# Optimization experiments

Hardware: AMD Instinct MI355X
Metric: run time of the kernel (lower is better)

The kernel has to match this reference:

```python
import jax, jax.numpy as jnp
import numpy as np
from jax import lax

B, IC, OC, H, W_DIM, K = 8, 64, 64, 256, 512, 3
BLUR_1D = [1.0, 3.0, 3.0, 1.0]
FACTOR = 2
GAIN = 1.0


def _blur_kernel():
    # setup_resample_kernel: outer product of 1D kernel, normalized to sum 1
    k = np.asarray(BLUR_1D, dtype=np.float32)
    k = np.outer(k, k)
    k = k / np.sum(k)
    return k  # [4,4]


def setup_inputs() -> dict:
    key = jax.random.key(0)
    ks = jax.random.split(key, 5)
    x = jax.random.normal(ks[0], (B, IC, H, H), dtype=jnp.float32)
    w = jax.random.normal(ks[1], (B, W_DIM), dtype=jnp.float32)
    # init_std = 1.0 for both weights since lrmul = 1.0
    w_conv = jax.random.normal(ks[2], (K, K, IC, OC), dtype=jnp.float32)
    w_dense = jax.random.normal(ks[3], (W_DIM, IC), dtype=jnp.float32)
    b_mod = jnp.zeros((IC,), dtype=jnp.float32)
    return {"x": x, "w": w, "w_conv": w_conv, "w_dense": w_dense, "b_mod": b_mod}


def reference(x, w, w_conv, w_dense, b_mod):
    k = w_conv.shape[0]
    ic, oc = w_conv.shape[2], w_conv.shape[3]

    # runtime coefs (equalized lr): he_std = gain / sqrt(fan_in), lrmul = 1
    coef_conv = 1.0 / np.sqrt(k * k * ic)
    coef_dense = 1.0 / np.sqrt(w.shape[1])

    # style = Dense(w) + bias (linear act, gain 1) + 1.0   -> [B, IC]
    style = w @ (coef_dense * w_dense) + b_mod + 1.0

    # modulate: [B,k,k,IC,OC]
    wmod = (coef_conv * w_conv)[None] * style[:, None, None, :, None]
    # demodulate over (kh, kw, ic)
    d = lax.rsqrt(jnp.sum(jnp.square(wmod), axis=(1, 2, 3)) + 1e-8)  # [B,OC]
    wmod = wmod * d[:, None, None, None, :]

    # per-sample grouped transposed conv (upsample x2) == lhs-dilated cross-corr
    # with the unflipped modulated weight, padding k-1 on each side.
    w_oihw = jnp.transpose(wmod, (0, 4, 3, 1, 2))  # [B,OC,IC,k,k]

    def up_conv(xb, wb):
        return lax.conv_general_dilated(
            xb[None], wb, window_strides=(1, 1),
            padding=[(k - 1, k - 1), (k - 1, k - 1)],
            lhs_dilation=(FACTOR, FACTOR),
            dimension_numbers=("NCHW", "OIHW", "NCHW"))[0]

    y = jax.vmap(up_conv)(x, w_oihw)  # [B,OC,(H-1)*2+k,(W-1)*2+k] = [B,OC,513,513]

    # upfirdn blur: kernel scaled by gain * factor**2, pad0 = pad1 = 1,
    # true convolution (kernel flipped in reference) applied depthwise.
    kb = jnp.asarray(_blur_kernel() * (GAIN * FACTOR ** 2))  # [4,4]
    fw = kb[::-1, ::-1][None, None]  # [1,1,4,4]
    b_, c_, s1, s2 = y.shape
    y = lax.conv_general_dilated(
        y.reshape(b_ * c_, 1, s1, s2), fw, window_strides=(1, 1),
        padding=[(1, 1), (1, 1)],
        dimension_numbers=("NCHW", "OIHW", "NCHW"))
    # output spatial: s1 + 2 - 4 + 1 = 2H
    return y.reshape(b_, c_, y.shape[2], y.shape[3])
```

## Files before the change

### kernel.cpp

```cpp
#include <hip/hip_runtime.h>

#define NB 8
#define IC 64
#define OC 64
#define HH 256
#define WD 512
#define PP 258

typedef __bf16 bf16x8 __attribute__((ext_vector_type(8)));
typedef float f32x16 __attribute__((ext_vector_type(16)));
typedef float f32x2 __attribute__((ext_vector_type(2)));

__device__ inline void compute_E(const float* __restrict__ w_conv, float stv,
                                 int oc, float E[6][6]) {
  const float coef_conv = 1.0f / 24.0f;
  const float s = stv * coef_conv;
  const int ic = threadIdx.x & 63;

  float wm[3][3];
  float ssq = 0.f;
  #pragma unroll
  for (int kh = 0; kh < 3; ++kh)
    #pragma unroll
    for (int kw = 0; kw < 3; ++kw) {
      float v = w_conv[((kh * 3 + kw) * IC + ic) * OC + oc] * s;
      wm[kh][kw] = v;
      ssq += v * v;
    }
  #pragma unroll
  for (int off = 32; off > 0; off >>= 1) ssq += __shfl_xor(ssq, off);
  const float d = rsqrtf(ssq + 1e-8f);
  #pragma unroll
  for (int kh = 0; kh < 3; ++kh)
    #pragma unroll
    for (int kw = 0; kw < 3; ++kw) wm[kh][kw] *= d;

  const float g[4] = {0.25f, 0.75f, 0.75f, 0.25f};
  #pragma unroll
  for (int a = 0; a < 6; ++a)
    #pragma unroll
    for (int c = 0; c < 6; ++c) {
      float acc = 0.f;
      #pragma unroll
      for (int dh = 0; dh < 3; ++dh) {
        int u = a - dh;
        if (u < 0 || u > 3) continue;
        #pragma unroll
        for (int dw = 0; dw < 3; ++dw) {
          int v = c - dw;
          if (v < 0 || v > 3) continue;
          acc = fmaf(wm[dh][dw], g[u] * g[v], acc);
        }
      }
      E[a][c] = acc;
    }
}

__device__ inline float style_of(const float* __restrict__ w,
                                 const float* __restrict__ w_dense,
                                 const float* __restrict__ b_mod, int b,
                                 int ic) {
  const float coef_dense = 0.044194173824159216f;
  const float* wr = w + b * WD;
  float acc = 0.f;
  for (int k = 0; k < WD; ++k) acc = fmaf(wr[k], w_dense[k * IC + ic], acc);
  return acc * coef_dense + b_mod[ic] + 1.0f;
}

__global__ __launch_bounds__(64) void pwfs_kernel(
    const float* __restrict__ w, const float* __restrict__ w_dense,
    const float* __restrict__ b_mod, const float* __restrict__ w_conv,
    __bf16* __restrict__ PWf) {
  const int oc = blockIdx.x;
  const int b = blockIdx.y;
  const int ic = threadIdx.x;

  float stv = style_of(w, w_dense, b_mod, b, ic);
  float E[6][6];
  compute_E(w_conv, stv, oc, E);

  const int ks = ic >> 4;
  const int h = (ic >> 3) & 1;
  const int e = ic & 7;
  const int lane = (oc & 31) + 32 * h;
  const int ocg = oc >> 5;

  #pragma unroll
  for (int pp = 0; pp < 2; ++pp)
    #pragma unroll
    for (int pq = 0; pq < 2; ++pq) {
      const int ph = pp * 2 + pq;
      #pragma unroll
      for (int j = 0; j < 3; ++j)
        #pragma unroll
        for (int l = 0; l < 3; ++l) {
          const int tap = j * 3 + l;
          float val = E[2 * j + 1 - pp][2 * l + 1 - pq];
          size_t off =
              ((size_t)(((((b * 4 + ph) * 9 + tap) * 2 + ocg) * 4 + ks)) * 64 +
               lane) * 8 + e;
          PWf[off] = (__bf16)val;
        }
    }
}

#define XS 268
__global__ __launch_bounds__(256) void xtp_kernel(const float* __restrict__ x,
                                                  __bf16* __restrict__ xTg) {
  __shared__ unsigned short buf[64 * XS];
  const int tid = threadIdx.x;
  const int m = blockIdx.x;
  const int b = blockIdx.y;

  if (m == 256) {
    uint4 z = make_uint4(0, 0, 0, 0);
    for (int i = tid; i < 8224; i += 256) {
      int pix = i >> 3;
      int sub = i & 7;
      int pr, pc;
      if (pix < 258) {
        pr = 0; pc = pix;
      } else if (pix < 516) {
        pr = 257; pc = pix - 258;
      } else {
        int rem = pix - 516;
        pr = 1 + (rem >> 1);
        pc = (rem & 1) ? 257 : 0;
      }
      *(uint4*)(xTg + ((size_t)(b * PP + pr) * PP + pc) * 64 + sub * 8) = z;
    }
    return;
  }

  const int ln = tid & 63, grp = tid >> 6;
  #pragma unroll
  for (int p = 0; p < 16; ++p) {
    const int ic = p * 4 + grp;
    float4 v = *(const float4*)(x + ((size_t)(b * 64 + ic) * 256 + m) * 256 +
                                ln * 4);
    ushort4 u4;
    u4.x = __builtin_bit_cast(unsigned short, (__bf16)v.x);
    u4.y = __builtin_bit_cast(unsigned short, (__bf16)v.y);
    u4.z = __builtin_bit_cast(unsigned short, (__bf16)v.z);
    u4.w = __builtin_bit_cast(unsigned short, (__bf16)v.w);
    *(ushort4*)&buf[ic * XS + ln * 4] = u4;
  }
  __syncthreads();
  #pragma unroll
  for (int it = 0; it < 8; ++it) {
    int pix = it * 32 + (tid >> 3);
    int g = tid & 7;
    bf16x8 o;
    #pragma unroll
    for (int e = 0; e < 8; ++e)
      o[e] = __builtin_bit_cast(__bf16, buf[(g * 8 + e) * XS + pix]);
    *(bf16x8*)(xTg + ((size_t)(b * PP + m + 1) * PP + (pix + 1)) * 64 +
               g * 8) = o;
  }
}

#define CMT 16
#define CNT 32
#define XR 18
#define XC 34

__device__ __forceinline__ void loadA(const bf16x8* __restrict__ Av, int phb,
                                      int ocg, int ks, int l, int lane,
                                      bf16x8 A[3][2]) {
  #pragma unroll
  for (int j = 0; j < 3; ++j) {
    const int tap = j * 3 + l;
    #pragma unroll
    for (int pq = 0; pq < 2; ++pq)
      A[j][pq] =
          Av[(size_t)((((phb + pq) * 9 + tap) * 2 + ocg) * 4 + ks) * 64 + lane];
  }
}

#define GLD_LDS(src, dst)                                                \
  __builtin_amdgcn_global_load_lds(                                      \
      (const __attribute__((address_space(1))) void*)(src),              \
      (__attribute__((address_space(3))) void*)(dst), 16, 0, 0)

__device__ __forceinline__ void stage_tile(const __bf16* __restrict__ xTg,
                                           int b, int m0, int n0,
                                           __bf16* xsbuf, int wv, int lane) {
  const int r0 = (18 * wv) >> 4;
  const int r1 = (18 * (wv + 1)) >> 4;
  for (int row = r0; row < r1; ++row) {
    const size_t srow = (size_t)(b * PP + m0 + row) * PP;
    __bf16* ldsrow = xsbuf + row * (XC * 64);
    #pragma unroll
    for (int q = 0; q < 4; ++q) {
      int pix = q * 8 + (lane >> 3);
      int g = (lane & 7) ^ (pix & 7);
      const __bf16* src = xTg + (srow + (n0 + pix)) * 64 + g * 8;
      GLD_LDS(src, ldsrow + q * 512);
    }
    if (lane < 16) {
      int pix = 32 + (lane >> 3);
      int g = (lane & 7) ^ (pix & 7);
      const __bf16* src = xTg + (srow + (n0 + pix)) * 64 + g * 8;
      GLD_LDS(src, ldsrow + 2048);
    }
  }
}

__global__ __launch_bounds__(1024) void conv32p_kernel(
    const __bf16* __restrict__ xTg, const __bf16* __restrict__ PWf,
    float* __restrict__ out) {
  __shared__ __bf16 xs[2][XR * XC * 64];

  const int tid = threadIdx.x;
  const int lane = tid & 63;
  const int wv = tid >> 6;
  const int pp = wv & 1;
  const int rh = wv >> 1;

  const int bid = blockIdx.x;
  const int ngrp = bid & 1;
  const int mtile = (bid >> 1) & 15;
  const int ocg = (bid >> 5) & 1;
  const int b = bid >> 6;
  const int m0 = mtile * CMT;

  const int ln31 = lane & 31;
  const int lh = lane >> 5;
  const bf16x8* Av = (const bf16x8*)PWf;
  const int phb = b * 4 + pp * 2;

  stage_tile(xTg, b, m0, ngrp * 128, &xs[0][0], wv, lane);
  asm volatile("s_waitcnt vmcnt(0)" ::: "memory");
  __builtin_amdgcn_s_barrier();

  #pragma unroll 1
  for (int t = 0; t < 4; ++t) {
    const int n0 = ngrp * 128 + t * 32;
    if (t < 3)
      stage_tile(xTg, b, m0, n0 + 32, &xs[(t + 1) & 1][0], wv, lane);

    const __bf16* xb = &xs[t & 1][0];

    f32x16 acc[2][2];
    #pragma unroll
    for (int mw = 0; mw < 2; ++mw)
      #pragma unroll
      for (int pq = 0; pq < 2; ++pq)
        #pragma unroll
        for (int e = 0; e < 16; ++e) acc[mw][pq][e] = 0.f;

    int ks = 0, l = 0;
    #pragma unroll 1
    for (int it = 0; it < 12; ++it) {
      bf16x8 Ac[3][2];
      loadA(Av, phb, ocg, ks, l, lane, Ac);

      bf16x8 Bf[4];
      const int col_t = ln31 + l;
      const int gneed = ks * 2 + lh;
      #pragma unroll
      for (int r = 0; r < 4; ++r) {
        const int lds_row = 2 * rh + r;
        Bf[r] = *(const bf16x8*)(xb + ((lds_row * XC + col_t) * 8 +
                                       (gneed ^ (col_t & 7))) * 8);
      }

      __builtin_amdgcn_s_setprio(1);
      #pragma unroll
      for (int r = 0; r < 4; ++r) {
        #pragma unroll
        for (int j = 0; j < 3; ++j) {
          const int mw = r - j;
          if (mw == 0 || mw == 1) {
            acc[mw][0] = __builtin_amdgcn_mfma_f32_32x32x16_bf16(
                Ac[j][0], Bf[r], acc[mw][0], 0, 0, 0);
            acc[mw][1] = __builtin_amdgcn_mfma_f32_32x32x16_bf16(
                Ac[j][1], Bf[r], acc[mw][1], 0, 0, 0);
          }
        }
      }
      __builtin_amdgcn_s_setprio(0);

      l = (l == 2) ? 0 : l + 1;
      ks = (l == 0) ? (ks + 1) & 3 : ks;
    }

    #pragma unroll
    for (int mw = 0; mw < 2; ++mw) {
      const int p = 2 * (m0 + 2 * rh + mw) + pp;
      #pragma unroll
      for (int rr = 0; rr < 16; ++rr) {
        const int oc_loc = (rr & 3) + 8 * (rr >> 2) + 4 * lh;
        const int oc = ocg * 32 + oc_loc;
        size_t off =
            ((size_t)(b * 64 + oc) * 512 + p) * 512 + 2 * n0 + 2 * ln31;
        f32x2 v2;
        v2[0] = acc[mw][0][rr];
        v2[1] = acc[mw][1][rr];
        __builtin_nontemporal_store(v2, (f32x2*)(out + off));
      }
    }

    asm volatile("s_waitcnt vmcnt(63)" ::: "memory");
    __builtin_amdgcn_s_barrier();
  }
}

__global__ __launch_bounds__(64) void pw_kernel(
    const float* __restrict__ w, const float* __restrict__ w_dense,
    const float* __restrict__ b_mod, const float* __restrict__ w_conv,
    float* __restrict__ PW) {
  const int oc = blockIdx.x;
  const int b = blockIdx.y;
  const int ic = threadIdx.x;
  float stv = style_of(w, w_dense, b_mod, b, ic);
  float E[6][6];
  compute_E(w_conv, stv, oc, E);
  #pragma unroll
  for (int pp = 0; pp < 2; ++pp)
    #pragma unroll
    for (int pq = 0; pq < 2; ++pq)
      #pragma unroll
      for (int j = 0; j < 3; ++j)
        #pragma unroll
        for (int l = 0; l < 3; ++l)
          PW[(((size_t)((b * 4 + pp * 2 + pq) * OC + oc) * IC + ic) * 9) +
             j * 3 + l] = E[2 * j + 1 - pp][2 * l + 1 - pq];
}

#define MT 16
#define NT 64
#define ICC 8
#define XROWS 18
#define XCOLS 66
#define XSTRIDE 68

__global__ __launch_bounds__(256) void conv_kernel(
    const float* __restrict__ x, const float* __restrict__ PW,
    float* __restrict__ out) {
  __shared__ float lds_x[ICC][XROWS][XSTRIDE];
  __shared__ float lds_w[4][ICC][9][4];

  const int tid = threadIdx.x;
  const int tn = tid & 15;
  const int tm = tid >> 4;
  const int bx = blockIdx.x;
  const int ntile = bx & 3;
  const int mtile = bx >> 2;
  const int ocg = blockIdx.y;
  const int b = blockIdx.z;
  const int m0 = mtile * MT;
  const int n0 = ntile * NT;

  float acc[4][4][4];
  #pragma unroll
  for (int o = 0; o < 4; ++o)
    #pragma unroll
    for (int ph = 0; ph < 4; ++ph)
      #pragma unroll
      for (int s = 0; s < 4; ++s) acc[o][ph][s] = 0.f;

  for (int ic0 = 0; ic0 < IC; ic0 += ICC) {
    __syncthreads();
    for (int ici = 0; ici < ICC; ++ici) {
      const float* xsrc = x + (size_t)(b * IC + ic0 + ici) * HH * HH;
      for (int rc = tid; rc < XROWS * XCOLS; rc += 256) {
        int r = rc / XCOLS;
        int c = rc - r * XCOLS;
        int gr = m0 - 1 + r;
        int gc = n0 - 1 + c;
        float v = 0.f;
        if ((unsigned)gr < HH && (unsigned)gc < HH) v = xsrc[gr * HH + gc];
        lds_x[ici][r][c] = v;
      }
    }
    for (int idx = tid; idx < 4 * ICC * 9 * 4; idx += 256) {
      int o = idx / (ICC * 9 * 4);
      int rem = idx - o * (ICC * 9 * 4);
      int ici = rem / 36;
      int r2 = rem - ici * 36;
      int t = r2 >> 2;
      int ph = r2 & 3;
      lds_w[o][ici][t][ph] =
          PW[(((size_t)((b * 4 + ph) * OC + (ocg * 4 + o)) * IC +
               (ic0 + ici)) * 9) + t];
    }
    __syncthreads();
    for (int ici = 0; ici < ICC; ++ici) {
      #pragma unroll
      for (int j = 0; j < 3; ++j) {
        const float* xr = &lds_x[ici][tm + j][tn * 4];
        float4 a4 = *(const float4*)xr;
        float2 a2 = *(const float2*)(xr + 4);
        float xv[6] = {a4.x, a4.y, a4.z, a4.w, a2.x, a2.y};
        #pragma unroll
        for (int l = 0; l < 3; ++l) {
          #pragma unroll
          for (int o = 0; o < 4; ++o) {
            float4 wv = *(const float4*)&lds_w[o][ici][j * 3 + l][0];
            #pragma unroll
            for (int s = 0; s < 4; ++s) {
              acc[o][0][s] = fmaf(wv.x, xv[l + s], acc[o][0][s]);
              acc[o][1][s] = fmaf(wv.y, xv[l + s], acc[o][1][s]);
              acc[o][2][s] = fmaf(wv.z, xv[l + s], acc[o][2][s]);
              acc[o][3][s] = fmaf(wv.w, xv[l + s], acc[o][3][s]);
            }
          }
        }
      }
    }
  }

  #pragma unroll
  for (int o = 0; o < 4; ++o) {
    #pragma unroll
    for (int pp = 0; pp < 2; ++pp) {
      const int p = 2 * (m0 + tm) + pp;
      float* dst = out +
          (((size_t)(b * OC + ocg * 4 + o) * 512 + p) * 512) + 2 * n0 + 8 * tn;
      float4 v0 = make_float4(acc[o][pp * 2 + 0][0], acc[o][pp * 2 + 1][0],
                              acc[o][pp * 2 + 0][1], acc[o][pp * 2 + 1][1]);
      float4 v1 = make_float4(acc[o][pp * 2 + 0][2], acc[o][pp * 2 + 1][2],
                              acc[o][pp * 2 + 0][3], acc[o][pp * 2 + 1][3]);
      *(float4*)dst = v0;
      *(float4*)(dst + 4) = v1;
    }
  }
}

extern "C" void kernel_launch(void* const* d_in, const int* in_sizes, int n_in,
                              void* d_out, int out_size, void* d_ws,
                              size_t ws_size, hipStream_t stream) {
  const float* x = (const float*)d_in[0];
  const float* w = (const float*)d_in[1];
  const float* w_conv = (const float*)d_in[2];
  const float* w_dense = (const float*)d_in[3];
  const float* b_mod = (const float*)d_in[4];
  float* out = (float*)d_out;

  const size_t PWF_BYTES = (size_t)8 * 4 * 9 * 2 * 4 * 64 * 8 * 2;
  const size_t XTG_BYTES = (size_t)8 * PP * PP * 64 * 2;
  const size_t NEED_NEW = PWF_BYTES + XTG_BYTES;

  if (ws_size >= NEED_NEW) {
    __bf16* PWf = (__bf16*)d_ws;
    __bf16* xTg = (__bf16*)((char*)d_ws + PWF_BYTES);
    pwfs_kernel<<<dim3(OC, NB), 64, 0, stream>>>(w, w_dense, b_mod, w_conv,
                                                 PWf);
    xtp_kernel<<<dim3(257, NB), 256, 0, stream>>>(x, xTg);
    conv32p_kernel<<<dim3(512), 1024, 0, stream>>>(xTg, PWf, out);
  } else {
    float* PW = (float*)d_ws;
    pw_kernel<<<dim3(OC, NB), 64, 0, stream>>>(w, w_dense, b_mod, w_conv, PW);
    conv_kernel<<<dim3(64, 16, NB), 256, 0, stream>>>(x, PW, out);
  }
}
```

Before: 278.5 us.

## Split column phases across wave pairs with taller row tiles and LDS exchange

Each wave now owns a single column phase and four output rows instead of two phases and two rows, so the six LDS B fragments per step feed more MFMAs and fewer A fragments are loaded per wave. Blocks cover the full width (eight column tiles) and the grid is halved to 256 blocks. Because adjacent output columns now sit in partner waves, accumulators are swapped through LDS before the interleaved f32x2 stores. The extra barriers, the full vmcnt(0) drain each tile, and the lower block count may reduce overlap and occupancy.

```diff
diff --git a/kernel.cpp b/kernel.cpp
--- a/kernel.cpp
+++ b/kernel.cpp
@@ -9,6 +9,7 @@
 
 typedef __bf16 bf16x8 __attribute__((ext_vector_type(8)));
 typedef float f32x16 __attribute__((ext_vector_type(16)));
+typedef float f32x4 __attribute__((ext_vector_type(4)));
 typedef float f32x2 __attribute__((ext_vector_type(2)));
 
 __device__ inline void compute_E(const float* __restrict__ w_conv, float stv,
@@ -164,19 +165,6 @@
 #define XR 18
 #define XC 34
 
-__device__ __forceinline__ void loadA(const bf16x8* __restrict__ Av, int phb,
-                                      int ocg, int ks, int l, int lane,
-                                      bf16x8 A[3][2]) {
-  #pragma unroll
-  for (int j = 0; j < 3; ++j) {
-    const int tap = j * 3 + l;
-    #pragma unroll
-    for (int pq = 0; pq < 2; ++pq)
-      A[j][pq] =
-          Av[(size_t)((((phb + pq) * 9 + tap) * 2 + ocg) * 4 + ks) * 64 + lane];
-  }
-}
-
 #define GLD_LDS(src, dst)                                                \
   __builtin_amdgcn_global_load_lds(                                      \
       (const __attribute__((address_space(1))) void*)(src),              \
@@ -206,76 +194,75 @@
   }
 }
 
-__global__ __launch_bounds__(1024) void conv32p_kernel(
+__global__ __launch_bounds__(1024, 4) void conv32x_kernel(
     const __bf16* __restrict__ xTg, const __bf16* __restrict__ PWf,
     float* __restrict__ out) {
-  __shared__ __bf16 xs[2][XR * XC * 64];
+  __shared__ bf16x8 xs[2][XR * XC * 8];
 
   const int tid = threadIdx.x;
   const int lane = tid & 63;
   const int wv = tid >> 6;
-  const int pp = wv & 1;
-  const int rh = wv >> 1;
+  const int pq = wv & 1;
+  const int pp = (wv >> 1) & 1;
+  const int rh = wv >> 2;
 
   const int bid = blockIdx.x;
-  const int ngrp = bid & 1;
-  const int mtile = (bid >> 1) & 15;
-  const int ocg = (bid >> 5) & 1;
-  const int b = bid >> 6;
+  const int mtile = bid & 15;
+  const int ocg = (bid >> 4) & 1;
+  const int b = bid >> 5;
   const int m0 = mtile * CMT;
 
   const int ln31 = lane & 31;
   const int lh = lane >> 5;
-  const bf16x8* Av = (const bf16x8*)PWf;
-  const int phb = b * 4 + pp * 2;
-
-  stage_tile(xTg, b, m0, ngrp * 128, &xs[0][0], wv, lane);
+  const int ph = b * 4 + pp * 2 + pq;
+  const bf16x8* Awave = (const bf16x8*)PWf + ((size_t)ph * 72 + ocg * 4) * 64 +
+                        lane;
+
+  stage_tile(xTg, b, m0, 0, (__bf16*)&xs[0][0], wv, lane);
   asm volatile("s_waitcnt vmcnt(0)" ::: "memory");
   __builtin_amdgcn_s_barrier();
 
   #pragma unroll 1
-  for (int t = 0; t < 4; ++t) {
-    const int n0 = ngrp * 128 + t * 32;
-    if (t < 3)
-      stage_tile(xTg, b, m0, n0 + 32, &xs[(t + 1) & 1][0], wv, lane);
-
-    const __bf16* xb = &xs[t & 1][0];
-
-    f32x16 acc[2][2];
-    #pragma unroll
-    for (int mw = 0; mw < 2; ++mw)
-      #pragma unroll
-      for (int pq = 0; pq < 2; ++pq)
-        #pragma unroll
-        for (int e = 0; e < 16; ++e) acc[mw][pq][e] = 0.f;
+  for (int t = 0; t < 8; ++t) {
+    const int n0 = t * 32;
+    if (t < 7)
+      stage_tile(xTg, b, m0, n0 + 32, (__bf16*)&xs[(t + 1) & 1][0], wv, lane);
+
+    const __bf16* xb = (const __bf16*)&xs[t & 1][0];
+
+    f32x16 acc[4];
+    #pragma unroll
+    for (int mw = 0; mw < 4; ++mw)
+      #pragma unroll
+      for (int e = 0; e < 16; ++e) acc[mw][e] = 0.f;
 
     int ks = 0, l = 0;
     #pragma unroll 1
     for (int it = 0; it < 12; ++it) {
-      bf16x8 Ac[3][2];
-      loadA(Av, phb, ocg, ks, l, lane, Ac);
-
-      bf16x8 Bf[4];
+      bf16x8 A[3];
+      #pragma unroll
+      for (int j = 0; j < 3; ++j)
+        A[j] = Awave[((j * 3 + l) * 8 + ks) * 64];
+
+      bf16x8 Bf[6];
       const int col_t = ln31 + l;
       const int gneed = ks * 2 + lh;
       #pragma unroll
-      for (int r = 0; r < 4; ++r) {
-        const int lds_row = 2 * rh + r;
+      for (int r = 0; r < 6; ++r) {
+        const int lds_row = 4 * rh + r;
         Bf[r] = *(const bf16x8*)(xb + ((lds_row * XC + col_t) * 8 +
                                        (gneed ^ (col_t & 7))) * 8);
       }
 
       __builtin_amdgcn_s_setprio(1);
       #pragma unroll
-      for (int r = 0; r < 4; ++r) {
+      for (int r = 0; r < 6; ++r) {
         #pragma unroll
         for (int j = 0; j < 3; ++j) {
           const int mw = r - j;
-          if (mw == 0 || mw == 1) {
-            acc[mw][0] = __builtin_amdgcn_mfma_f32_32x32x16_bf16(
-                Ac[j][0], Bf[r], acc[mw][0], 0, 0, 0);
-            acc[mw][1] = __builtin_amdgcn_mfma_f32_32x32x16_bf16(
-                Ac[j][1], Bf[r], acc[mw][1], 0, 0, 0);
+          if (mw >= 0 && mw < 4) {
+            acc[mw] = __builtin_amdgcn_mfma_f32_32x32x16_bf16(A[j], Bf[r],
+                                                              acc[mw], 0, 0, 0);
           }
         }
       }
@@ -285,24 +272,55 @@
       ks = (l == 0) ? (ks + 1) & 3 : ks;
     }
 
-    #pragma unroll
-    for (int mw = 0; mw < 2; ++mw) {
-      const int p = 2 * (m0 + 2 * rh + mw) + pp;
-      #pragma unroll
-      for (int rr = 0; rr < 16; ++rr) {
-        const int oc_loc = (rr & 3) + 8 * (rr >> 2) + 4 * lh;
-        const int oc = ocg * 32 + oc_loc;
-        size_t off =
-            ((size_t)(b * 64 + oc) * 512 + p) * 512 + 2 * n0 + 2 * ln31;
-        f32x2 v2;
-        v2[0] = acc[mw][0][rr];
-        v2[1] = acc[mw][1][rr];
-        __builtin_nontemporal_store(v2, (f32x2*)(out + off));
-      }
-    }
-
-    asm volatile("s_waitcnt vmcnt(63)" ::: "memory");
+    asm volatile("s_waitcnt vmcnt(0)" ::: "memory");
     __builtin_amdgcn_s_barrier();
+
+    float* exb = (float*)&xs[t & 1][0];
+    #pragma unroll
+    for (int half = 0; half < 2; ++half) {
+      #pragma unroll
+      for (int mp = 0; mp < 2; ++mp) {
+        const int mw = half * 2 + mp;
+        #pragma unroll
+        for (int g = 0; g < 2; ++g) {
+          const int gg = (pq == 0) ? 2 + g : g;
+          f32x4 s;
+          #pragma unroll
+          for (int jj = 0; jj < 4; ++jj) s[jj] = acc[mw][gg * 4 + jj];
+          *(f32x4*)&exb[(((wv * 2 + mp) * 2 + g) * 64 + lane) * 4] = s;
+        }
+      }
+      __builtin_amdgcn_s_barrier();
+      #pragma unroll
+      for (int mp = 0; mp < 2; ++mp) {
+        const int mw = half * 2 + mp;
+        f32x4 po[2];
+        #pragma unroll
+        for (int g = 0; g < 2; ++g)
+          po[g] = *(const f32x4*)&exb[((((wv ^ 1) * 2 + mp) * 2 + g) * 64 +
+                                       lane) * 4];
+        const int p = 2 * (m0 + 4 * rh + mw) + pp;
+        #pragma unroll
+        for (int g = 0; g < 2; ++g) {
+          const int og = (pq == 0) ? g : 2 + g;
+          #pragma unroll
+          for (int jj = 0; jj < 4; ++jj) {
+            const int rr = og * 4 + jj;
+            const int oc_loc = (rr & 3) + 8 * (rr >> 2) + 4 * lh;
+            const int oc = ocg * 32 + oc_loc;
+            const float a_own = acc[mw][rr];
+            const float a_par = po[g][jj];
+            f32x2 v2;
+            v2[0] = (pq == 0) ? a_own : a_par;
+            v2[1] = (pq == 0) ? a_par : a_own;
+            size_t off =
+                ((size_t)(b * 64 + oc) * 512 + p) * 512 + 2 * n0 + 2 * ln31;
+            __builtin_nontemporal_store(v2, (f32x2*)(out + off));
+          }
+        }
+      }
+      __builtin_amdgcn_s_barrier();
+    }
   }
 }
 
@@ -448,7 +466,7 @@
     pwfs_kernel<<<dim3(OC, NB), 64, 0, stream>>>(w, w_dense, b_mod, w_conv,
                                                  PWf);
     xtp_kernel<<<dim3(257, NB), 256, 0, stream>>>(x, xTg);
-    conv32p_kernel<<<dim3(512), 1024, 0, stream>>>(xTg, PWf, out);
+    conv32x_kernel<<<dim3(256), 1024, 0, stream>>>(xTg, PWf, out);
   } else {
     float* PW = (float*)d_ws;
     pw_kernel<<<dim3(OC, NB), 64, 0, stream>>>(w, w_dense, b_mod, w_conv, PW);
```

Measured after the change: 357.4 us. 28.3% more time.

## Shrink conv blocks to 512 threads with single-buffered LDS tile for occupancy

Applied to the files above, without the earlier changes.

Changes the main conv kernel from 1024-thread blocks over 16 output rows with double-buffered LDS to 512-thread blocks over 8 rows with a single LDS buffer. Each block now sweeps all 8 column tiles instead of 4, and launch bounds request 4 blocks per CU. The aim is to raise occupancy and cut LDS footprint so several blocks can overlap each other's loads. In exchange, the prefetch pipelining inside a block is gone: each tile load is bracketed by two full barriers, and halo rows are re-read more often because the tiles are shorter.

```diff
diff --git a/kernel.cpp b/kernel.cpp
--- a/kernel.cpp
+++ b/kernel.cpp
@@ -159,9 +159,8 @@
   }
 }
 
-#define CMT 16
-#define CNT 32
-#define XR 18
+#define CMT 8
+#define XR 10
 #define XC 34
 
 __device__ __forceinline__ void loadA(const bf16x8* __restrict__ Av, int phb,
@@ -185,8 +184,8 @@
 __device__ __forceinline__ void stage_tile(const __bf16* __restrict__ xTg,
                                            int b, int m0, int n0,
                                            __bf16* xsbuf, int wv, int lane) {
-  const int r0 = (18 * wv) >> 4;
-  const int r1 = (18 * (wv + 1)) >> 4;
+  const int r0 = (XR * wv) >> 3;
+  const int r1 = (XR * (wv + 1)) >> 3;
   for (int row = r0; row < r1; ++row) {
     const size_t srow = (size_t)(b * PP + m0 + row) * PP;
     __bf16* ldsrow = xsbuf + row * (XC * 64);
@@ -206,10 +205,10 @@
   }
 }
 
-__global__ __launch_bounds__(1024) void conv32p_kernel(
+__global__ __launch_bounds__(512, 4) void conv32s_kernel(
     const __bf16* __restrict__ xTg, const __bf16* __restrict__ PWf,
     float* __restrict__ out) {
-  __shared__ __bf16 xs[2][XR * XC * 64];
+  __shared__ __bf16 xs[XR * XC * 64];
 
   const int tid = threadIdx.x;
   const int lane = tid & 63;
@@ -218,8 +217,7 @@
   const int rh = wv >> 1;
 
   const int bid = blockIdx.x;
-  const int ngrp = bid & 1;
-  const int mtile = (bid >> 1) & 15;
+  const int mtile = bid & 31;
   const int ocg = (bid >> 5) & 1;
   const int b = bid >> 6;
   const int m0 = mtile * CMT;
@@ -229,17 +227,12 @@
   const bf16x8* Av = (const bf16x8*)PWf;
   const int phb = b * 4 + pp * 2;
 
-  stage_tile(xTg, b, m0, ngrp * 128, &xs[0][0], wv, lane);
-  asm volatile("s_waitcnt vmcnt(0)" ::: "memory");
-  __builtin_amdgcn_s_barrier();
+  stage_tile(xTg, b, m0, 0, xs, wv, lane);
+  __syncthreads();
 
   #pragma unroll 1
-  for (int t = 0; t < 4; ++t) {
-    const int n0 = ngrp * 128 + t * 32;
-    if (t < 3)
-      stage_tile(xTg, b, m0, n0 + 32, &xs[(t + 1) & 1][0], wv, lane);
-
-    const __bf16* xb = &xs[t & 1][0];
+  for (int t = 0; t < 8; ++t) {
+    const int n0 = t * 32;
 
     f32x16 acc[2][2];
     #pragma unroll
@@ -261,7 +254,7 @@
       #pragma unroll
       for (int r = 0; r < 4; ++r) {
         const int lds_row = 2 * rh + r;
-        Bf[r] = *(const bf16x8*)(xb + ((lds_row * XC + col_t) * 8 +
+        Bf[r] = *(const bf16x8*)(xs + ((lds_row * XC + col_t) * 8 +
                                        (gneed ^ (col_t & 7))) * 8);
       }
 
@@ -301,8 +294,11 @@
       }
     }
 
-    asm volatile("s_waitcnt vmcnt(63)" ::: "memory");
-    __builtin_amdgcn_s_barrier();
+    if (t < 7) {
+      __syncthreads();
+      stage_tile(xTg, b, m0, n0 + 32, xs, wv, lane);
+      __syncthreads();
+    }
   }
 }
 
@@ -448,7 +444,7 @@
     pwfs_kernel<<<dim3(OC, NB), 64, 0, stream>>>(w, w_dense, b_mod, w_conv,
                                                  PWf);
     xtp_kernel<<<dim3(257, NB), 256, 0, stream>>>(x, xTg);
-    conv32p_kernel<<<dim3(512), 1024, 0, stream>>>(xTg, PWf, out);
+    conv32s_kernel<<<dim3(512), 512, 0, stream>>>(xTg, PWf, out);
   } else {
     float* PW = (float*)d_ws;
     pw_kernel<<<dim3(OC, NB), 64, 0, stream>>>(w, w_dense, b_mod, w_conv, PW);
```

Result: faster. 259.2 us (-6.9%).

## Retile conv into 4-row blocks covering both oc halves with smaller workgroups

Applied to the files above, without the earlier changes.

The main MFMA conv kernel moves from 1024-thread blocks over 16 rows by 128 columns for one oc half to 512-thread blocks over 4 rows by 256 columns. Each block now covers both oc halves (waves split by oc group), so the staged input tile is shared across all 64 output channels instead of being reloaded per half. Each wave stages one LDS row, the block index is swizzled across batches, and launch bounds allow up to 4 blocks per CU. The end-of-tile sync now waits for all memory ops before storing and drops the final barrier, which may cost some overlap, and the 6-row halo for every 4 output rows re-reads more input rows than before.

```diff
diff --git a/kernel.cpp b/kernel.cpp
--- a/kernel.cpp
+++ b/kernel.cpp
@@ -159,9 +159,8 @@
   }
 }
 
-#define CMT 16
-#define CNT 32
-#define XR 18
+#define CMT 4
+#define XR 6
 #define XC 34
 
 __device__ __forceinline__ void loadA(const bf16x8* __restrict__ Av, int phb,
@@ -182,12 +181,11 @@
       (const __attribute__((address_space(1))) void*)(src),              \
       (__attribute__((address_space(3))) void*)(dst), 16, 0, 0)
 
-__device__ __forceinline__ void stage_tile(const __bf16* __restrict__ xTg,
-                                           int b, int m0, int n0,
-                                           __bf16* xsbuf, int wv, int lane) {
-  const int r0 = (18 * wv) >> 4;
-  const int r1 = (18 * (wv + 1)) >> 4;
-  for (int row = r0; row < r1; ++row) {
+__device__ __forceinline__ void stage6(const __bf16* __restrict__ xTg, int b,
+                                       int m0, int n0, __bf16* xsbuf, int wv,
+                                       int lane) {
+  if (wv < XR) {
+    const int row = wv;
     const size_t srow = (size_t)(b * PP + m0 + row) * PP;
     __bf16* ldsrow = xsbuf + row * (XC * 64);
     #pragma unroll
@@ -206,7 +204,7 @@
   }
 }
 
-__global__ __launch_bounds__(1024) void conv32p_kernel(
+__global__ __launch_bounds__(512, 4) void conv32d_kernel(
     const __bf16* __restrict__ xTg, const __bf16* __restrict__ PWf,
     float* __restrict__ out) {
   __shared__ __bf16 xs[2][XR * XC * 64];
@@ -215,12 +213,12 @@
   const int lane = tid & 63;
   const int wv = tid >> 6;
   const int pp = wv & 1;
-  const int rh = wv >> 1;
-
-  const int bid = blockIdx.x;
-  const int ngrp = bid & 1;
-  const int mtile = (bid >> 1) & 15;
-  const int ocg = (bid >> 5) & 1;
+  const int og = (wv >> 1) & 1;
+  const int rh = wv >> 2;
+
+  const int raw = blockIdx.x;
+  const int bid = (raw & 7) * 64 + (raw >> 3);
+  const int mtile = bid & 63;
   const int b = bid >> 6;
   const int m0 = mtile * CMT;
 
@@ -229,15 +227,14 @@
   const bf16x8* Av = (const bf16x8*)PWf;
   const int phb = b * 4 + pp * 2;
 
-  stage_tile(xTg, b, m0, ngrp * 128, &xs[0][0], wv, lane);
+  stage6(xTg, b, m0, 0, &xs[0][0], wv, lane);
   asm volatile("s_waitcnt vmcnt(0)" ::: "memory");
   __builtin_amdgcn_s_barrier();
 
   #pragma unroll 1
-  for (int t = 0; t < 4; ++t) {
-    const int n0 = ngrp * 128 + t * 32;
-    if (t < 3)
-      stage_tile(xTg, b, m0, n0 + 32, &xs[(t + 1) & 1][0], wv, lane);
+  for (int t = 0; t < 8; ++t) {
+    const int n0 = t * 32;
+    if (t < 7) stage6(xTg, b, m0, n0 + 32, &xs[(t + 1) & 1][0], wv, lane);
 
     const __bf16* xb = &xs[t & 1][0];
 
@@ -253,7 +250,7 @@
     #pragma unroll 1
     for (int it = 0; it < 12; ++it) {
       bf16x8 Ac[3][2];
-      loadA(Av, phb, ocg, ks, l, lane, Ac);
+      loadA(Av, phb, og, ks, l, lane, Ac);
 
       bf16x8 Bf[4];
       const int col_t = ln31 + l;
@@ -285,13 +282,15 @@
       ks = (l == 0) ? (ks + 1) & 3 : ks;
     }
 
+    asm volatile("s_waitcnt vmcnt(0)" ::: "memory");
+
     #pragma unroll
     for (int mw = 0; mw < 2; ++mw) {
       const int p = 2 * (m0 + 2 * rh + mw) + pp;
       #pragma unroll
       for (int rr = 0; rr < 16; ++rr) {
         const int oc_loc = (rr & 3) + 8 * (rr >> 2) + 4 * lh;
-        const int oc = ocg * 32 + oc_loc;
+        const int oc = og * 32 + oc_loc;
         size_t off =
             ((size_t)(b * 64 + oc) * 512 + p) * 512 + 2 * n0 + 2 * ln31;
         f32x2 v2;
@@ -301,8 +300,7 @@
       }
     }
 
-    asm volatile("s_waitcnt vmcnt(63)" ::: "memory");
-    __builtin_amdgcn_s_barrier();
+    if (t < 7) __builtin_amdgcn_s_barrier();
   }
 }
 
@@ -448,7 +446,7 @@
     pwfs_kernel<<<dim3(OC, NB), 64, 0, stream>>>(w, w_dense, b_mod, w_conv,
                                                  PWf);
     xtp_kernel<<<dim3(257, NB), 256, 0, stream>>>(x, xTg);
-    conv32p_kernel<<<dim3(512), 1024, 0, stream>>>(xTg, PWf, out);
+    conv32d_kernel<<<dim3(512), 512, 0, stream>>>(xTg, PWf, out);
   } else {
     float* PW = (float*)d_ws;
     pw_kernel<<<dim3(OC, NB), 64, 0, stream>>>(w, w_dense, b_mod, w_conv, PW);
```

Result: faster. 260.8 us (-6.3%).
